# Kernel tuning notes

Measured on AMD Instinct MI355X. Metric: run time of the kernel, lower is better.

The kernel has to match this reference:

```python
import jax, jax.numpy as jnp
import numpy as np

N = 50000      # nodes
E = 800000     # edges
IN = 128       # in_channels
HID = 128      # hidden_channels
OUT = 2        # out_channels (edge classes)
HEADS = 8      # EGConv default num_heads
BASES = 4      # EGConv default num_bases
FH = HID // HEADS  # per-head feature dim = 16


def _egconv(x, Wb, Wc, bc, b, row, col, norm, n):
    """One EGConv layer (aggregators=['symnorm']), self-loops already in row/col/norm.
    Wb: [in, BASES*FH] basis projection (no bias).
    Wc: [in, HEADS*BASES], bc: combination weights linear.
    b : [HID] output bias.
    """
    bases = x @ Wb                                            # [n, BASES*FH]
    msg = bases[row] * norm[:, None]                          # gather + symnorm scale
    agg = jax.ops.segment_sum(msg, col, num_segments=n)       # scatter-add -> [n, BASES*FH]
    w = (x @ Wc + bc).reshape(n, HEADS, BASES)                # per-node combination weights
    out = jnp.einsum('nhb,nbf->nhf', w, agg.reshape(n, BASES, FH))
    return out.reshape(n, HEADS * FH) + b


def setup_inputs() -> dict:
    key = jax.random.key(0)
    ks = jax.random.split(key, 12)
    s = 0.05
    inp = {
        'x': jax.random.normal(ks[0], (N, IN), jnp.float32),
        'edge_index': jax.random.randint(ks[1], (2, E), 0, N, jnp.int64),
        # conv1
        'Wb1': jax.random.normal(ks[2], (IN, BASES * FH), jnp.float32) * s,
        'Wc1': jax.random.normal(ks[3], (IN, HEADS * BASES), jnp.float32) * s,
        'bc1': jnp.zeros((HEADS * BASES,), jnp.float32),
        'b1': jnp.zeros((HID,), jnp.float32),
        # conv2
        'Wb2': jax.random.normal(ks[4], (HID, BASES * FH), jnp.float32) * s,
        'Wc2': jax.random.normal(ks[5], (HID, HEADS * BASES), jnp.float32) * s,
        'bc2': jnp.zeros((HEADS * BASES,), jnp.float32),
        'b2': jnp.zeros((HID,), jnp.float32),
        # edge classifier
        'Wcls': jax.random.normal(ks[6], (2 * HID, OUT), jnp.float32) * s,
        'bcls': jnp.zeros((OUT,), jnp.float32),
    }
    return inp


def reference(x, edge_index, Wb1, Wc1, bc1, b1, Wb2, Wc2, bc2, b2, Wcls, bcls):
    n = x.shape[0]
    # add self loops (EGConv default add_self_loops=True) + gcn_norm symnorm weights
    sl = jnp.arange(n, dtype=edge_index.dtype)
    row = jnp.concatenate([edge_index[0], sl])
    col = jnp.concatenate([edge_index[1], sl])
    deg = jax.ops.segment_sum(jnp.ones(row.shape[0], x.dtype), col, num_segments=n)
    dis = jnp.where(deg > 0, deg, 1.0) ** -0.5
    dis = jnp.where(deg > 0, dis, 0.0)
    norm = dis[row] * dis[col]                                # symnorm edge weight

    h = jax.nn.relu(_egconv(x, Wb1, Wc1, bc1, b1, row, col, norm, n))
    h = _egconv(h, Wb2, Wc2, bc2, b2, row, col, norm, n)

    # edge classifier: gather endpoint embeddings of ORIGINAL edges, concat, linear
    e = jnp.concatenate([h[edge_index[0]], h[edge_index[1]]], axis=-1)  # [E, 2*HID]
    return e @ Wcls + bcls
```

## Files before the change

kernel.cpp:

```cpp
#include <hip/hip_runtime.h>
#include <hip/hip_fp16.h>

#define NN 50000
#define EE 800000
#define NB_E2 1563
#define WIN 6250
#define EPB 1024
#define NCHUNK 782

__global__ void k_count(const int* __restrict__ ei, int* cnt, int* __restrict__ rank) {
    int t = blockIdx.x * 256 + threadIdx.x;
    if (t < EE / 2) {
        int2 cc = *(const int2*)(ei + EE + 2 * t);
        int r0 = atomicAdd(&cnt[cc.x], 1);
        int r1 = atomicAdd(&cnt[cc.y], 1);
        *(int2*)(rank + 2 * t) = make_int2(r0, r1);
    }
}

__global__ void k_scan1(const int* __restrict__ cnt, int* sloc, int* bsum,
                        float* dis, int n) {
    __shared__ int s[256];
    int tid = threadIdx.x;
    int i = blockIdx.x * 256 + tid;
    int v = (i < n) ? cnt[i] : 0;
    if (i < n) dis[i] = rsqrtf((float)v + 1.0f);
    s[tid] = v;
    __syncthreads();
    for (int off = 1; off < 256; off <<= 1) {
        int t2 = 0;
        if (tid >= off) t2 = s[tid - off];
        __syncthreads();
        if (tid >= off) s[tid] += t2;
        __syncthreads();
    }
    if (i < n) sloc[i] = s[tid] - v;
    if (tid == 255) bsum[blockIdx.x] = s[255];
}

__global__ void k_scan23(const int* __restrict__ sloc, const int* __restrict__ bsum,
                         const int* __restrict__ cnt, int2* sd, int* starts,
                         int n, int nb) {
    __shared__ int sb[256];
    int tid = threadIdx.x, b = blockIdx.x;
    int v = (tid < nb && tid < b) ? bsum[tid] : 0;
    sb[tid] = v;
    __syncthreads();
    for (int off = 128; off; off >>= 1) {
        if (tid < off) sb[tid] += sb[tid + off];
        __syncthreads();
    }
    int boff = sb[0];
    int i = b * 256 + tid;
    if (i < n) {
        int st = sloc[i] + boff;
        sd[i] = make_int2(st, cnt[i]);
        starts[i] = st;
    }
}

__global__ __launch_bounds__(256) void k_fill(
    const int* __restrict__ ei, const int* __restrict__ rank,
    const int* __restrict__ starts, int* __restrict__ csr)
{
    int w = blockIdx.x & 7;
    int chunk = blockIdx.x >> 3;
    int base = chunk * EPB + threadIdx.x * 4;
    int lo = w * WIN, hi = lo + WIN;
    if (base + 3 < EE) {
        int4 rr = *(const int4*)(ei + base);
        int4 cc = *(const int4*)(ei + EE + base);
        int4 rk = *(const int4*)(rank + base);
        if (cc.x >= lo && cc.x < hi) csr[starts[cc.x] + rk.x] = rr.x;
        if (cc.y >= lo && cc.y < hi) csr[starts[cc.y] + rk.y] = rr.y;
        if (cc.z >= lo && cc.z < hi) csr[starts[cc.z] + rk.z] = rr.z;
        if (cc.w >= lo && cc.w < hi) csr[starts[cc.w] + rk.w] = rr.w;
    } else {
        for (int e = 0; e < 4; e++) {
            int t = base + e;
            if (t < EE) {
                int c = ei[EE + t];
                if (c >= lo && c < hi) csr[starts[c] + rank[t]] = ei[t];
            }
        }
    }
}

__global__ __launch_bounds__(256) void k_gemm(
    const float* __restrict__ x, const float* __restrict__ Wb,
    const float* __restrict__ Wc, const float* __restrict__ bc,
    const float* __restrict__ dis,
    __half* __restrict__ bsh, float* __restrict__ wcomb, int n)
{
    __shared__ float xt[32 * 257];
    int tid = threadIdx.x;
    int grp = blockIdx.y;
    int row0 = blockIdx.x * 256;
    int row = row0 + tid;
    bool valid = row < n;

    const float* W = (grp < 2) ? (Wb + grp * 32) : Wc;
    const int ldw = (grp < 2) ? 64 : 32;

    float acc[32];
#pragma unroll
    for (int c = 0; c < 32; c++) acc[c] = 0.f;

    for (int s = 0; s < 4; s++) {
        int base_k = s * 32;
        float4 v[8];
#pragma unroll
        for (int i = 0; i < 8; i++) {
            int idx = i * 256 + tid;
            int r = idx >> 3;
            int k4 = idx & 7;
            int gr = row0 + r;
            v[i] = (gr < n) ? *(const float4*)(x + (size_t)gr * 128 + base_k + k4 * 4)
                            : make_float4(0.f, 0.f, 0.f, 0.f);
        }
        __syncthreads();
#pragma unroll
        for (int i = 0; i < 8; i++) {
            int idx = i * 256 + tid;
            int r = idx >> 3;
            int k4 = idx & 7;
            xt[(k4 * 4 + 0) * 257 + r] = v[i].x;
            xt[(k4 * 4 + 1) * 257 + r] = v[i].y;
            xt[(k4 * 4 + 2) * 257 + r] = v[i].z;
            xt[(k4 * 4 + 3) * 257 + r] = v[i].w;
        }
        __syncthreads();

        const float* Ws = W + base_k * ldw;
#pragma unroll 8
        for (int k = 0; k < 32; k++) {
            float xs = xt[k * 257 + tid];
            const float* wk = Ws + k * ldw;
#pragma unroll
            for (int c = 0; c < 32; c++) acc[c] = fmaf(xs, wk[c], acc[c]);
        }
    }

    if (!valid) return;
    if (grp < 2) {
        float d = dis[row];
        __half2 hh[16];
#pragma unroll
        for (int c = 0; c < 16; c++)
            hh[c] = __floats2half2_rn(acc[2 * c] * d, acc[2 * c + 1] * d);
        uint4* bo = (uint4*)(bsh + (size_t)row * 64 + grp * 32);
        const uint4* src = (const uint4*)hh;
#pragma unroll
        for (int c = 0; c < 4; c++) bo[c] = src[c];
    } else {
        float4* wo = (float4*)(wcomb + (size_t)row * 32);
#pragma unroll
        for (int c = 0; c < 8; c++)
            wo[c] = make_float4(acc[4*c] + bc[4*c], acc[4*c+1] + bc[4*c+1],
                                acc[4*c+2] + bc[4*c+2], acc[4*c+3] + bc[4*c+3]);
    }
}

template<int LAYER2>
__global__ __launch_bounds__(256) void k_agg(
    const int* __restrict__ csr, const int2* __restrict__ sd,
    const __half* __restrict__ bsh, const float* __restrict__ dis,
    const float* __restrict__ wcomb, const float* __restrict__ bias,
    float* __restrict__ h,
    const float* __restrict__ Wcls, const float* __restrict__ bcls,
    float* __restrict__ p, int n)
{
    int wid = (blockIdx.x * 256 + threadIdx.x) >> 6;
    int lane = threadIdx.x & 63;
    if (wid >= n) return;
    int2 s2 = sd[wid];
    int start = s2.x, deg = s2.y;
    int g = lane >> 4, q = lane & 15;

    const uint2* bsp = (const uint2*)bsh;
    float4 acc4 = make_float4(0.f, 0.f, 0.f, 0.f);
    if (g == 0) {
        uint2 v = bsp[(size_t)wid * 16 + q];
        float2 lo = __half22float2(*(const __half2*)&v.x);
        float2 hi = __half22float2(*(const __half2*)&v.y);
        acc4 = make_float4(lo.x, lo.y, hi.x, hi.y);
    }

    int j = 0;
    int ia = 0, ib = 0;
    if (8 <= deg) { ia = csr[start + g]; ib = csr[start + 4 + g]; }
    while (j + 8 <= deg) {
        int jn = j + 8;
        int na = 0, nb = 0;
        if (jn + 8 <= deg) { na = csr[start + jn + g]; nb = csr[start + jn + 4 + g]; }
        uint2 v0 = bsp[(size_t)ia * 16 + q];
        uint2 v1 = bsp[(size_t)ib * 16 + q];
        float2 l0 = __half22float2(*(const __half2*)&v0.x);
        float2 h0 = __half22float2(*(const __half2*)&v0.y);
        float2 l1 = __half22float2(*(const __half2*)&v1.x);
        float2 h1 = __half22float2(*(const __half2*)&v1.y);
        acc4.x += l0.x + l1.x;
        acc4.y += l0.y + l1.y;
        acc4.z += h0.x + h1.x;
        acc4.w += h0.y + h1.y;
        ia = na; ib = nb; j = jn;
    }
    int last = start + deg - 1;
    for (; j < deg; j += 4) {
        int idx = start + j + g;
        int r = csr[min(idx, last)];
        uint2 v = bsp[(size_t)r * 16 + q];
        float2 lo = __half22float2(*(const __half2*)&v.x);
        float2 hi = __half22float2(*(const __half2*)&v.y);
        float m = (j + g < deg) ? 1.f : 0.f;
        acc4.x = fmaf(lo.x, m, acc4.x);
        acc4.y = fmaf(lo.y, m, acc4.y);
        acc4.z = fmaf(hi.x, m, acc4.z);
        acc4.w = fmaf(hi.y, m, acc4.w);
    }

    acc4.x += __shfl_xor(acc4.x, 16, 64);
    acc4.y += __shfl_xor(acc4.y, 16, 64);
    acc4.z += __shfl_xor(acc4.z, 16, 64);
    acc4.w += __shfl_xor(acc4.w, 16, 64);
    acc4.x += __shfl_xor(acc4.x, 32, 64);
    acc4.y += __shfl_xor(acc4.y, 32, 64);
    acc4.z += __shfl_xor(acc4.z, 32, 64);
    acc4.w += __shfl_xor(acc4.w, 32, 64);

    float d = dis[wid];
    acc4.x *= d; acc4.y *= d; acc4.z *= d; acc4.w *= d;

    int src = lane >> 2;
    float t0 = __shfl(acc4.x, src, 64);
    float t1 = __shfl(acc4.y, src, 64);
    float t2 = __shfl(acc4.z, src, 64);
    float t3 = __shfl(acc4.w, src, 64);
    int c = lane & 3;
    float acc = (c == 0) ? t0 : (c == 1) ? t1 : (c == 2) ? t2 : t3;

    int fh = lane & 15;
    float a0 = __shfl(acc, fh, 64);
    float a1 = __shfl(acc, 16 + fh, 64);
    float a2 = __shfl(acc, 32 + fh, 64);
    float a3 = __shfl(acc, 48 + fh, 64);
    const float* wn = wcomb + (size_t)wid * 32;
    int hd = lane >> 4;
    float s1 = bias[lane];
    float s2v = bias[64 + lane];
    s1 = fmaf(wn[hd * 4 + 0], a0, s1);
    s1 = fmaf(wn[hd * 4 + 1], a1, s1);
    s1 = fmaf(wn[hd * 4 + 2], a2, s1);
    s1 = fmaf(wn[hd * 4 + 3], a3, s1);
    s2v = fmaf(wn[(4 + hd) * 4 + 0], a0, s2v);
    s2v = fmaf(wn[(4 + hd) * 4 + 1], a1, s2v);
    s2v = fmaf(wn[(4 + hd) * 4 + 2], a2, s2v);
    s2v = fmaf(wn[(4 + hd) * 4 + 3], a3, s2v);

    if (!LAYER2) {
        s1 = fmaxf(s1, 0.f);
        s2v = fmaxf(s2v, 0.f);
        h[(size_t)wid * 128 + lane] = s1;
        h[(size_t)wid * 128 + 64 + lane] = s2v;
    } else {
        float r0 = s1 * Wcls[lane * 2 + 0] + s2v * Wcls[(64 + lane) * 2 + 0];
        float r1 = s1 * Wcls[lane * 2 + 1] + s2v * Wcls[(64 + lane) * 2 + 1];
        float r2 = s1 * Wcls[(128 + lane) * 2 + 0] + s2v * Wcls[(192 + lane) * 2 + 0];
        float r3 = s1 * Wcls[(128 + lane) * 2 + 1] + s2v * Wcls[(192 + lane) * 2 + 1];
#pragma unroll
        for (int off = 32; off; off >>= 1) {
            r0 += __shfl_xor(r0, off, 64);
            r1 += __shfl_xor(r1, off, 64);
            r2 += __shfl_xor(r2, off, 64);
            r3 += __shfl_xor(r3, off, 64);
        }
        if (lane == 0) {
            p[wid * 4 + 0] = r0 + bcls[0];
            p[wid * 4 + 1] = r1 + bcls[1];
            p[wid * 4 + 2] = r2;
            p[wid * 4 + 3] = r3;
        }
    }
}

__global__ void k_edge(const int* __restrict__ ei, const float* __restrict__ p,
                       float* __restrict__ out)
{
    int t = blockIdx.x * blockDim.x + threadIdx.x;
    if (t >= EE / 2) return;
    int2 rr = *(const int2*)(ei + 2 * t);
    int2 cc = *(const int2*)(ei + EE + 2 * t);
    float2 pt0 = *(const float2*)(p + rr.x * 4);
    float2 pt1 = *(const float2*)(p + rr.y * 4);
    float2 pb0 = *(const float2*)(p + cc.x * 4 + 2);
    float2 pb1 = *(const float2*)(p + cc.y * 4 + 2);
    float4 o;
    o.x = pt0.x + pb0.x;
    o.y = pt0.y + pb0.y;
    o.z = pt1.x + pb1.x;
    o.w = pt1.y + pb1.y;
    *(float4*)(out + (size_t)t * 4) = o;
}

extern "C" void kernel_launch(void* const* d_in, const int* in_sizes, int n_in,
                              void* d_out, int out_size, void* d_ws, size_t ws_size,
                              hipStream_t stream) {
    const float* x    = (const float*)d_in[0];
    const int*   ei   = (const int*)d_in[1];
    const float* Wb1  = (const float*)d_in[2];
    const float* Wc1  = (const float*)d_in[3];
    const float* bc1  = (const float*)d_in[4];
    const float* b1   = (const float*)d_in[5];
    const float* Wb2  = (const float*)d_in[6];
    const float* Wc2  = (const float*)d_in[7];
    const float* bc2  = (const float*)d_in[8];
    const float* b2   = (const float*)d_in[9];
    const float* Wcls = (const float*)d_in[10];
    const float* bcls = (const float*)d_in[11];
    float* out = (float*)d_out;

    char* ws = (char*)d_ws;
    size_t off = 0;
    auto alloc = [&](size_t bytes) {
        void* pp = ws + off;
        off += (bytes + 15) & ~(size_t)15;
        return pp;
    };

    float*  dis    = (float*)alloc(50048 * 4);
    __half* bsh    = (__half*)alloc((size_t)NN * 64 * 2);
    float*  wcomb  = (float*)alloc((size_t)NN * 32 * 4);
    float*  h      = (float*)alloc((size_t)NN * 128 * 4);
    float*  p      = (float*)alloc((size_t)NN * 4 * 4);
    int*    cnt    = (int*)alloc(50048 * 4);
    int*    sloc   = (int*)alloc(50048 * 4);
    int*    starts = (int*)alloc(50048 * 4);
    int*    bsum   = (int*)alloc(256 * 4);
    int2*   sd     = (int2*)alloc((size_t)50048 * 8);
    int*    csr    = (int*)alloc((size_t)EE * 4);
    int*    rank   = (int*)alloc((size_t)EE * 4);

    const int B = 256;
    int gN   = (NN + B - 1) / B;
    int gN64 = (NN * 64) / B;
    dim3 gG(gN, 3);

    hipMemsetAsync(cnt, 0, NN * sizeof(int), stream);
    k_count<<<NB_E2, B, 0, stream>>>(ei, cnt, rank);
    k_scan1<<<gN, B, 0, stream>>>(cnt, sloc, bsum, dis, NN);
    k_scan23<<<gN, B, 0, stream>>>(sloc, bsum, cnt, sd, starts, NN, gN);
    k_fill<<<NCHUNK * 8, B, 0, stream>>>(ei, rank, starts, csr);

    k_gemm<<<gG, B, 0, stream>>>(x, Wb1, Wc1, bc1, dis, bsh, wcomb, NN);
    k_agg<0><<<gN64, B, 0, stream>>>(csr, sd, bsh, dis, wcomb, b1, h,
                                     Wcls, bcls, p, NN);

    k_gemm<<<gG, B, 0, stream>>>(h, Wb2, Wc2, bc2, dis, bsh, wcomb, NN);
    k_agg<1><<<gN64, B, 0, stream>>>(csr, sd, bsh, dis, wcomb, b2, h,
                                     Wcls, bcls, p, NN);

    k_edge<<<NB_E2, B, 0, stream>>>(ei, p, out);
}
```

Measured before the change: 277.7 us.

## Bucket CSR neighbors by source window to improve gather locality

Counts edges per (destination, source-window) bucket instead of per destination, so each node's neighbor list in the CSR is grouped by source index range. Degrees and normalization are derived from bucket starts inside the fill kernel, and the scans now run with 1024-thread blocks over the larger bucket array. The aim is more cache-friendly gathers of source features during aggregation, at the cost of an 8x larger counter array, memset and scan.

```diff
diff --git a/kernel.cpp b/kernel.cpp
--- a/kernel.cpp
+++ b/kernel.cpp
@@ -4,30 +4,36 @@
 #define NN 50000
 #define EE 800000
 #define NB_E2 1563
+#define NWIN 8
 #define WIN 6250
+#define NBUCK (NN * NWIN)
 #define EPB 1024
 #define NCHUNK 782
+#define NSD 196
+#define NSB 391
 
 __global__ void k_count(const int* __restrict__ ei, int* cnt, int* __restrict__ rank) {
     int t = blockIdx.x * 256 + threadIdx.x;
     if (t < EE / 2) {
+        int2 rr = *(const int2*)(ei + 2 * t);
         int2 cc = *(const int2*)(ei + EE + 2 * t);
-        int r0 = atomicAdd(&cnt[cc.x], 1);
-        int r1 = atomicAdd(&cnt[cc.y], 1);
+        int b0 = cc.x * NWIN + rr.x / WIN;
+        int b1 = cc.y * NWIN + rr.y / WIN;
+        int r0 = atomicAdd(&cnt[b0], 1);
+        int r1 = atomicAdd(&cnt[b1], 1);
         *(int2*)(rank + 2 * t) = make_int2(r0, r1);
     }
 }
 
-__global__ void k_scan1(const int* __restrict__ cnt, int* sloc, int* bsum,
-                        float* dis, int n) {
-    __shared__ int s[256];
+__global__ __launch_bounds__(1024) void k_scan1(
+    const int* __restrict__ cnt, int* sloc, int* bsum, int n) {
+    __shared__ int s[1024];
     int tid = threadIdx.x;
-    int i = blockIdx.x * 256 + tid;
+    int i = blockIdx.x * 1024 + tid;
     int v = (i < n) ? cnt[i] : 0;
-    if (i < n) dis[i] = rsqrtf((float)v + 1.0f);
     s[tid] = v;
     __syncthreads();
-    for (int off = 1; off < 256; off <<= 1) {
+    for (int off = 1; off < 1024; off <<= 1) {
         int t2 = 0;
         if (tid >= off) t2 = s[tid - off];
         __syncthreads();
@@ -35,52 +41,62 @@
         __syncthreads();
     }
     if (i < n) sloc[i] = s[tid] - v;
-    if (tid == 255) bsum[blockIdx.x] = s[255];
-}
-
-__global__ void k_scan23(const int* __restrict__ sloc, const int* __restrict__ bsum,
-                         const int* __restrict__ cnt, int2* sd, int* starts,
-                         int n, int nb) {
-    __shared__ int sb[256];
+    if (tid == 1023) bsum[blockIdx.x] = s[1023];
+}
+
+__global__ __launch_bounds__(1024) void k_scan23(
+    const int* __restrict__ sloc, const int* __restrict__ bsum,
+    int* bstart, int n, int nb) {
+    __shared__ int sb[1024];
     int tid = threadIdx.x, b = blockIdx.x;
     int v = (tid < nb && tid < b) ? bsum[tid] : 0;
     sb[tid] = v;
     __syncthreads();
-    for (int off = 128; off; off >>= 1) {
+    for (int off = 512; off; off >>= 1) {
         if (tid < off) sb[tid] += sb[tid + off];
         __syncthreads();
     }
     int boff = sb[0];
-    int i = b * 256 + tid;
-    if (i < n) {
-        int st = sloc[i] + boff;
-        sd[i] = make_int2(st, cnt[i]);
-        starts[i] = st;
-    }
+    int i = b * 1024 + tid;
+    if (i < n) bstart[i] = sloc[i] + boff;
 }
 
 __global__ __launch_bounds__(256) void k_fill(
     const int* __restrict__ ei, const int* __restrict__ rank,
-    const int* __restrict__ starts, int* __restrict__ csr)
+    const int* __restrict__ bstart, int* __restrict__ csr,
+    int2* __restrict__ sd, float* __restrict__ dis)
 {
-    int w = blockIdx.x & 7;
-    int chunk = blockIdx.x >> 3;
+    int b = blockIdx.x;
+    if (b >= NCHUNK * 8) {
+        int i = (b - NCHUNK * 8) * 256 + threadIdx.x;
+        if (i < NN) {
+            int st = bstart[i * NWIN];
+            int end = (i + 1 < NN) ? bstart[i * NWIN + NWIN] : EE;
+            int deg = end - st;
+            sd[i] = make_int2(st, deg);
+            dis[i] = rsqrtf((float)deg + 1.0f);
+        }
+        return;
+    }
+    int w = b & 7;
+    int chunk = b >> 3;
     int base = chunk * EPB + threadIdx.x * 4;
     int lo = w * WIN, hi = lo + WIN;
     if (base + 3 < EE) {
         int4 rr = *(const int4*)(ei + base);
         int4 cc = *(const int4*)(ei + EE + base);
         int4 rk = *(const int4*)(rank + base);
-        if (cc.x >= lo && cc.x < hi) csr[starts[cc.x] + rk.x] = rr.x;
-        if (cc.y >= lo && cc.y < hi) csr[starts[cc.y] + rk.y] = rr.y;
-        if (cc.z >= lo && cc.z < hi) csr[starts[cc.z] + rk.z] = rr.z;
-        if (cc.w >= lo && cc.w < hi) csr[starts[cc.w] + rk.w] = rr.w;
+        if (cc.x >= lo && cc.x < hi) csr[bstart[cc.x * NWIN + rr.x / WIN] + rk.x] = rr.x;
+        if (cc.y >= lo && cc.y < hi) csr[bstart[cc.y * NWIN + rr.y / WIN] + rk.y] = rr.y;
+        if (cc.z >= lo && cc.z < hi) csr[bstart[cc.z * NWIN + rr.z / WIN] + rk.z] = rr.z;
+        if (cc.w >= lo && cc.w < hi) csr[bstart[cc.w * NWIN + rr.w / WIN] + rk.w] = rr.w;
     } else {
         for (int e = 0; e < 4; e++) {
             int t = base + e;
             if (t < EE) {
                 int c = ei[EE + t];
-                if (c >= lo && c < hi) csr[starts[c] + rank[t]] = ei[t];
+                int r = ei[t];
+                if (c >= lo && c < hi) csr[bstart[c * NWIN + r / WIN] + rank[t]] = r;
             }
         }
     }
@@ -332,10 +348,10 @@
     float*  wcomb  = (float*)alloc((size_t)NN * 32 * 4);
     float*  h      = (float*)alloc((size_t)NN * 128 * 4);
     float*  p      = (float*)alloc((size_t)NN * 4 * 4);
-    int*    cnt    = (int*)alloc(50048 * 4);
-    int*    sloc   = (int*)alloc(50048 * 4);
-    int*    starts = (int*)alloc(50048 * 4);
-    int*    bsum   = (int*)alloc(256 * 4);
+    int*    cnt    = (int*)alloc((size_t)NBUCK * 4);
+    int*    sloc   = (int*)alloc((size_t)NBUCK * 4);
+    int*    bstart = (int*)alloc((size_t)(NBUCK + 16) * 4);
+    int*    bsum   = (int*)alloc(1024 * 4);
     int2*   sd     = (int2*)alloc((size_t)50048 * 8);
     int*    csr    = (int*)alloc((size_t)EE * 4);
     int*    rank   = (int*)alloc((size_t)EE * 4);
@@ -345,11 +361,11 @@
     int gN64 = (NN * 64) / B;
     dim3 gG(gN, 3);
 
-    hipMemsetAsync(cnt, 0, NN * sizeof(int), stream);
+    hipMemsetAsync(cnt, 0, (size_t)NBUCK * sizeof(int), stream);
     k_count<<<NB_E2, B, 0, stream>>>(ei, cnt, rank);
-    k_scan1<<<gN, B, 0, stream>>>(cnt, sloc, bsum, dis, NN);
-    k_scan23<<<gN, B, 0, stream>>>(sloc, bsum, cnt, sd, starts, NN, gN);
-    k_fill<<<NCHUNK * 8, B, 0, stream>>>(ei, rank, starts, csr);
+    k_scan1<<<NSB, 1024, 0, stream>>>(cnt, sloc, bsum, NBUCK);
+    k_scan23<<<NSB, 1024, 0, stream>>>(sloc, bsum, bstart, NBUCK, NSB);
+    k_fill<<<NCHUNK * 8 + NSD, B, 0, stream>>>(ei, rank, bstart, csr, sd, dis);
 
     k_gemm<<<gG, B, 0, stream>>>(x, Wb1, Wc1, bc1, dis, bsh, wcomb, NN);
     k_agg<0><<<gN64, B, 0, stream>>>(csr, sd, bsh, dis, wcomb, b1, h,
```

Result: no change. 280.2 us (+0.9%).

## Fuse CSR fill with layer-1 GEMM and widen aggregation gathers to 16-byte loads

Applied to the files above, without the earlier changes.

Merges the CSR fill kernel and the first projection GEMM into one launch, with the block index choosing which job a block does, so the two independent stages overlap and one launch is dropped. The aggregation kernel is rewritten so each wave loads 64 neighbor indices at once, hands them out by shuffle, and gathers 8 halves (16 bytes) per lane. Eight neighbors are now processed per step instead of four, and the self-loop term is added after the reduction. The fused kernel requires the large shared buffer even for fill blocks, which may lower occupancy for those blocks, and the wider gather uses more registers.

```diff
diff --git a/kernel.cpp b/kernel.cpp
--- a/kernel.cpp
+++ b/kernel.cpp
@@ -4,9 +4,12 @@
 #define NN 50000
 #define EE 800000
 #define NB_E2 1563
+#define NWIN 8
 #define WIN 6250
 #define EPB 1024
 #define NCHUNK 782
+#define NFILL (NCHUNK * 8)
+#define NGX 196
 
 __global__ void k_count(const int* __restrict__ ei, int* cnt, int* __restrict__ rank) {
     int t = blockIdx.x * 256 + threadIdx.x;
@@ -59,43 +62,14 @@
     }
 }
 
-__global__ __launch_bounds__(256) void k_fill(
-    const int* __restrict__ ei, const int* __restrict__ rank,
-    const int* __restrict__ starts, int* __restrict__ csr)
-{
-    int w = blockIdx.x & 7;
-    int chunk = blockIdx.x >> 3;
-    int base = chunk * EPB + threadIdx.x * 4;
-    int lo = w * WIN, hi = lo + WIN;
-    if (base + 3 < EE) {
-        int4 rr = *(const int4*)(ei + base);
-        int4 cc = *(const int4*)(ei + EE + base);
-        int4 rk = *(const int4*)(rank + base);
-        if (cc.x >= lo && cc.x < hi) csr[starts[cc.x] + rk.x] = rr.x;
-        if (cc.y >= lo && cc.y < hi) csr[starts[cc.y] + rk.y] = rr.y;
-        if (cc.z >= lo && cc.z < hi) csr[starts[cc.z] + rk.z] = rr.z;
-        if (cc.w >= lo && cc.w < hi) csr[starts[cc.w] + rk.w] = rr.w;
-    } else {
-        for (int e = 0; e < 4; e++) {
-            int t = base + e;
-            if (t < EE) {
-                int c = ei[EE + t];
-                if (c >= lo && c < hi) csr[starts[c] + rank[t]] = ei[t];
-            }
-        }
-    }
-}
-
-__global__ __launch_bounds__(256) void k_gemm(
+__device__ __forceinline__ void gemm_body(
+    int bx, int grp, int tid, float* xt,
     const float* __restrict__ x, const float* __restrict__ Wb,
     const float* __restrict__ Wc, const float* __restrict__ bc,
     const float* __restrict__ dis,
     __half* __restrict__ bsh, float* __restrict__ wcomb, int n)
 {
-    __shared__ float xt[32 * 257];
-    int tid = threadIdx.x;
-    int grp = blockIdx.y;
-    int row0 = blockIdx.x * 256;
+    int row0 = bx * 256;
     int row = row0 + tid;
     bool valid = row < n;
 
@@ -161,6 +135,66 @@
     }
 }
 
+__global__ __launch_bounds__(256) void k_fill_gemm(
+    const int* __restrict__ ei, const int* __restrict__ rank,
+    const int* __restrict__ starts, int* __restrict__ csr,
+    const float* __restrict__ x, const float* __restrict__ Wb,
+    const float* __restrict__ Wc, const float* __restrict__ bc,
+    const float* __restrict__ dis,
+    __half* __restrict__ bsh, float* __restrict__ wcomb, int n)
+{
+    __shared__ float xt[32 * 257];
+    int b = blockIdx.x;
+    if (b < NFILL) {
+        int w = b & 7;
+        int chunk = b >> 3;
+        int base = chunk * EPB + threadIdx.x * 4;
+        int lo = w * WIN, hi = lo + WIN;
+        if (base + 3 < EE) {
+            int4 rr = *(const int4*)(ei + base);
+            int4 cc = *(const int4*)(ei + EE + base);
+            int4 rk = *(const int4*)(rank + base);
+            if (cc.x >= lo && cc.x < hi) csr[starts[cc.x] + rk.x] = rr.x;
+            if (cc.y >= lo && cc.y < hi) csr[starts[cc.y] + rk.y] = rr.y;
+            if (cc.z >= lo && cc.z < hi) csr[starts[cc.z] + rk.z] = rr.z;
+            if (cc.w >= lo && cc.w < hi) csr[starts[cc.w] + rk.w] = rr.w;
+        } else {
+            for (int e = 0; e < 4; e++) {
+                int t = base + e;
+                if (t < EE) {
+                    int c = ei[EE + t];
+                    if (c >= lo && c < hi) csr[starts[c] + rank[t]] = ei[t];
+                }
+            }
+        }
+        return;
+    }
+    int bb = b - NFILL;
+    int grp = bb / NGX;
+    int bx = bb - grp * NGX;
+    gemm_body(bx, grp, threadIdx.x, xt, x, Wb, Wc, bc, dis, bsh, wcomb, n);
+}
+
+__global__ __launch_bounds__(256) void k_gemm(
+    const float* __restrict__ x, const float* __restrict__ Wb,
+    const float* __restrict__ Wc, const float* __restrict__ bc,
+    const float* __restrict__ dis,
+    __half* __restrict__ bsh, float* __restrict__ wcomb, int n)
+{
+    __shared__ float xt[32 * 257];
+    gemm_body(blockIdx.x, blockIdx.y, threadIdx.x, xt, x, Wb, Wc, bc, dis,
+              bsh, wcomb, n);
+}
+
+__device__ __forceinline__ void h8_to_f8(uint4 v, float* f) {
+    float2 a = __half22float2(*(const __half2*)&v.x);
+    float2 b = __half22float2(*(const __half2*)&v.y);
+    float2 c = __half22float2(*(const __half2*)&v.z);
+    float2 d = __half22float2(*(const __half2*)&v.w);
+    f[0] = a.x; f[1] = a.y; f[2] = b.x; f[3] = b.y;
+    f[4] = c.x; f[5] = c.y; f[6] = d.x; f[7] = d.y;
+}
+
 template<int LAYER2>
 __global__ __launch_bounds__(256) void k_agg(
     const int* __restrict__ csr, const int2* __restrict__ sd,
@@ -175,75 +209,71 @@
     if (wid >= n) return;
     int2 s2 = sd[wid];
     int start = s2.x, deg = s2.y;
-    int g = lane >> 4, q = lane & 15;
-
-    const uint2* bsp = (const uint2*)bsh;
-    float4 acc4 = make_float4(0.f, 0.f, 0.f, 0.f);
-    if (g == 0) {
-        uint2 v = bsp[(size_t)wid * 16 + q];
-        float2 lo = __half22float2(*(const __half2*)&v.x);
-        float2 hi = __half22float2(*(const __half2*)&v.y);
-        acc4 = make_float4(lo.x, lo.y, hi.x, hi.y);
-    }
-
-    int j = 0;
-    int ia = 0, ib = 0;
-    if (8 <= deg) { ia = csr[start + g]; ib = csr[start + 4 + g]; }
-    while (j + 8 <= deg) {
-        int jn = j + 8;
-        int na = 0, nb = 0;
-        if (jn + 8 <= deg) { na = csr[start + jn + g]; nb = csr[start + jn + 4 + g]; }
-        uint2 v0 = bsp[(size_t)ia * 16 + q];
-        uint2 v1 = bsp[(size_t)ib * 16 + q];
-        float2 l0 = __half22float2(*(const __half2*)&v0.x);
-        float2 h0 = __half22float2(*(const __half2*)&v0.y);
-        float2 l1 = __half22float2(*(const __half2*)&v1.x);
-        float2 h1 = __half22float2(*(const __half2*)&v1.y);
-        acc4.x += l0.x + l1.x;
-        acc4.y += l0.y + l1.y;
-        acc4.z += h0.x + h1.x;
-        acc4.w += h0.y + h1.y;
-        ia = na; ib = nb; j = jn;
-    }
-    int last = start + deg - 1;
-    for (; j < deg; j += 4) {
-        int idx = start + j + g;
-        int r = csr[min(idx, last)];
-        uint2 v = bsp[(size_t)r * 16 + q];
-        float2 lo = __half22float2(*(const __half2*)&v.x);
-        float2 hi = __half22float2(*(const __half2*)&v.y);
-        float m = (j + g < deg) ? 1.f : 0.f;
-        acc4.x = fmaf(lo.x, m, acc4.x);
-        acc4.y = fmaf(lo.y, m, acc4.y);
-        acc4.z = fmaf(hi.x, m, acc4.z);
-        acc4.w = fmaf(hi.y, m, acc4.w);
-    }
-
-    acc4.x += __shfl_xor(acc4.x, 16, 64);
-    acc4.y += __shfl_xor(acc4.y, 16, 64);
-    acc4.z += __shfl_xor(acc4.z, 16, 64);
-    acc4.w += __shfl_xor(acc4.w, 16, 64);
-    acc4.x += __shfl_xor(acc4.x, 32, 64);
-    acc4.y += __shfl_xor(acc4.y, 32, 64);
-    acc4.z += __shfl_xor(acc4.z, 32, 64);
-    acc4.w += __shfl_xor(acc4.w, 32, 64);
-
+    int g = lane >> 3, q = lane & 7;
+    const uint4* bsp4 = (const uint4*)bsh;
+
+    float acc[8];
+#pragma unroll
+    for (int j = 0; j < 8; j++) acc[j] = 0.f;
+
+    int nw = (deg + 63) >> 6;
+    for (int wdw = 0; wdw < nw; wdw++) {
+        int wb = wdw << 6;
+        int rem = min(deg - wb, 64);
+        int idxv = (lane < rem) ? csr[start + wb + lane] : 0;
+        int e0 = 0;
+        for (; e0 + 16 <= rem; e0 += 16) {
+            int r0 = __shfl(idxv, e0 + g, 64);
+            int r1 = __shfl(idxv, e0 + 8 + g, 64);
+            uint4 v0 = bsp4[(size_t)r0 * 8 + q];
+            uint4 v1 = bsp4[(size_t)r1 * 8 + q];
+            float f0[8], f1[8];
+            h8_to_f8(v0, f0);
+            h8_to_f8(v1, f1);
+#pragma unroll
+            for (int j = 0; j < 8; j++) acc[j] += f0[j] + f1[j];
+        }
+        for (; e0 < rem; e0 += 8) {
+            int r = __shfl(idxv, e0 + g, 64);
+            float m = (e0 + g < rem) ? 1.f : 0.f;
+            uint4 v = bsp4[(size_t)r * 8 + q];
+            float f[8];
+            h8_to_f8(v, f);
+#pragma unroll
+            for (int j = 0; j < 8; j++) acc[j] = fmaf(f[j], m, acc[j]);
+        }
+    }
+
+#pragma unroll
+    for (int off = 8; off <= 32; off <<= 1)
+#pragma unroll
+        for (int j = 0; j < 8; j++) acc[j] += __shfl_xor(acc[j], off, 64);
+
+    uint4 sv = bsp4[(size_t)wid * 8 + q];
+    float sf[8];
+    h8_to_f8(sv, sf);
     float d = dis[wid];
-    acc4.x *= d; acc4.y *= d; acc4.z *= d; acc4.w *= d;
-
-    int src = lane >> 2;
-    float t0 = __shfl(acc4.x, src, 64);
-    float t1 = __shfl(acc4.y, src, 64);
-    float t2 = __shfl(acc4.z, src, 64);
-    float t3 = __shfl(acc4.w, src, 64);
-    int c = lane & 3;
-    float acc = (c == 0) ? t0 : (c == 1) ? t1 : (c == 2) ? t2 : t3;
+#pragma unroll
+    for (int j = 0; j < 8; j++) acc[j] = (acc[j] + sf[j]) * d;
+
+    int srcq = lane >> 3;
+    float v0 = __shfl(acc[0], srcq, 64);
+    float v1 = __shfl(acc[1], srcq, 64);
+    float v2 = __shfl(acc[2], srcq, 64);
+    float v3 = __shfl(acc[3], srcq, 64);
+    float v4 = __shfl(acc[4], srcq, 64);
+    float v5 = __shfl(acc[5], srcq, 64);
+    float v6 = __shfl(acc[6], srcq, 64);
+    float v7 = __shfl(acc[7], srcq, 64);
+    int jj = lane & 7;
+    float a = (jj == 0) ? v0 : (jj == 1) ? v1 : (jj == 2) ? v2 : (jj == 3) ? v3
+            : (jj == 4) ? v4 : (jj == 5) ? v5 : (jj == 6) ? v6 : v7;
 
     int fh = lane & 15;
-    float a0 = __shfl(acc, fh, 64);
-    float a1 = __shfl(acc, 16 + fh, 64);
-    float a2 = __shfl(acc, 32 + fh, 64);
-    float a3 = __shfl(acc, 48 + fh, 64);
+    float a0 = __shfl(a, fh, 64);
+    float a1 = __shfl(a, 16 + fh, 64);
+    float a2 = __shfl(a, 32 + fh, 64);
+    float a3 = __shfl(a, 48 + fh, 64);
     const float* wn = wcomb + (size_t)wid * 32;
     int hd = lane >> 4;
     float s1 = bias[lane];
@@ -343,15 +373,15 @@
     const int B = 256;
     int gN   = (NN + B - 1) / B;
     int gN64 = (NN * 64) / B;
-    dim3 gG(gN, 3);
+    dim3 gG(NGX, 3);
 
     hipMemsetAsync(cnt, 0, NN * sizeof(int), stream);
     k_count<<<NB_E2, B, 0, stream>>>(ei, cnt, rank);
     k_scan1<<<gN, B, 0, stream>>>(cnt, sloc, bsum, dis, NN);
     k_scan23<<<gN, B, 0, stream>>>(sloc, bsum, cnt, sd, starts, NN, gN);
-    k_fill<<<NCHUNK * 8, B, 0, stream>>>(ei, rank, starts, csr);
-
-    k_gemm<<<gG, B, 0, stream>>>(x, Wb1, Wc1, bc1, dis, bsh, wcomb, NN);
+
+    k_fill_gemm<<<NFILL + NGX * 3, B, 0, stream>>>(
+        ei, rank, starts, csr, x, Wb1, Wc1, bc1, dis, bsh, wcomb, NN);
     k_agg<0><<<gN64, B, 0, stream>>>(csr, sd, bsh, dis, wcomb, b1, h,
                                      Wcls, bcls, p, NN);
 
```

After: 282.0 us. Within noise of the previous version (+1.6%).
